# Performance work log

Measured on AMD Instinct MI355X. Metric: run time of the kernel, lower is better.

Reference implementation:

```python
import jax, jax.numpy as jnp
import numpy as np

B, T, C, H = 4, 2048, 1024, 16
HD = C // H


def setup_inputs() -> dict:
    key = jax.random.key(0)
    kx, kq, ko = jax.random.split(key, 3)
    x = jax.random.normal(kx, (B, T, C), dtype=jnp.float32)
    # torch nn.Linear weight layout: [out_features, in_features]
    wqkv = jax.random.normal(kq, (3 * C, C), dtype=jnp.float32) * (1.0 / np.sqrt(C))
    wo = jax.random.normal(ko, (C, C), dtype=jnp.float32) * (1.0 / np.sqrt(C))
    return {"x": x, "wqkv": wqkv, "wo": wo}


def reference(x, wqkv, wo):
    Bn, Tn, Cn = x.shape
    # fused QKV projection: x @ wqkv.T -> [B, T, 3C]
    qkv = jnp.einsum('btc,dc->btd', x, wqkv)
    qkv = qkv.reshape(Bn, Tn, 3, H, HD)
    q = qkv[:, :, 0].transpose(0, 2, 1, 3)  # [B, H, T, hd]
    k = qkv[:, :, 1].transpose(0, 2, 1, 3)
    v = qkv[:, :, 2].transpose(0, 2, 1, 3)
    scale = 1.0 / np.sqrt(HD).astype(np.float32)
    scores = jnp.einsum('bhqd,bhkd->bhqk', q, k) * scale  # [B, H, T, T]
    causal = jnp.tril(jnp.ones((Tn, Tn), dtype=bool))
    scores = jnp.where(causal, scores, jnp.finfo(scores.dtype).min)
    attn = jax.nn.softmax(scores, axis=-1)
    y = jnp.einsum('bhqk,bhkd->bhqd', attn, v)  # [B, H, T, hd]
    y = y.transpose(0, 2, 1, 3).reshape(Bn, Tn, Cn)
    return jnp.einsum('btc,dc->btd', y, wo)
```

## Files before the change

### kernel.cpp

```cpp
#include <hip/hip_runtime.h>
#include <hip/hip_bf16.h>
#include <stdint.h>


typedef __attribute__((ext_vector_type(8))) short short8;
typedef __attribute__((ext_vector_type(4))) float f32x4;
typedef __attribute__((ext_vector_type(4))) float float4v;
typedef __attribute__((ext_vector_type(4))) unsigned short ushort4v;
typedef __attribute__((ext_vector_type(4))) unsigned int u32x4;

#define AS1 __attribute__((address_space(1)))
#define AS3 __attribute__((address_space(3)))

#if __has_builtin(__builtin_amdgcn_exp2f)
#define EXP2(x) __builtin_amdgcn_exp2f(x)
#else
#define EXP2(x) __expf((x) * 0.69314718f)
#endif

static __device__ __forceinline__ void gload_lds16(const void* g, void* l) {
  __builtin_amdgcn_global_load_lds((const AS1 void*)g, (AS3 void*)l, 16, 0, 0);
}

__global__ void k_detect(const unsigned int* __restrict__ x, int* __restrict__ flag) {
  __shared__ int sm[256];
  int c = 0;
  for (int i = 0; i < 8; ++i) {
    unsigned int v = x[threadIdx.x * 8 + i];
    unsigned int e = (v >> 7) & 0xffu;
    if (e >= 110u && e <= 140u) c++;
  }
  sm[threadIdx.x] = c;
  __syncthreads();
  if (threadIdx.x == 0) {
    int t = 0;
    for (int i = 0; i < 256; ++i) t += sm[i];
    *flag = (t > 1024) ? 1 : 0;
  }
}

__global__ void k_convert3(const void* __restrict__ xs, const void* __restrict__ wqs,
                           const void* __restrict__ wos, unsigned short* __restrict__ out,
                           const int* __restrict__ flag) {
  const int f = *flag;
  const int stride = gridDim.x * blockDim.x;
  for (int v = blockIdx.x * blockDim.x + threadIdx.x; v < 3145728; v += stride) {
    const int i = v * 4;
    const void* src; int j;
    if (i < 8388608)        { src = xs;  j = i; }
    else if (i < 11534336)  { src = wqs; j = i - 8388608; }
    else                    { src = wos; j = i - 11534336; }
    ushort4v r;
    if (f) {
      r = *(const ushort4v*)((const unsigned short*)src + j);
    } else {
      float4v fv = *(const float4v*)((const float*)src + j);
#pragma unroll
      for (int e = 0; e < 4; e++) {
        __hip_bfloat16 h = __float2bfloat16(fv[e]);
        r[e] = *(unsigned short*)&h;
      }
    }
    *(ushort4v*)(out + i) = r;
  }
}

__global__ __launch_bounds__(256) void k_gemm_qkv(
    const __hip_bfloat16* __restrict__ X, const __hip_bfloat16* __restrict__ W,
    __hip_bfloat16* __restrict__ qo, __hip_bfloat16* __restrict__ ko,
    __hip_bfloat16* __restrict__ vto) {
  __shared__ __align__(16) __hip_bfloat16 As[128 * 32];
  __shared__ __align__(16) __hip_bfloat16 Bs[128 * 32];
  const int tid = threadIdx.x;
  const int lane = tid & 63;
  const int wid = tid >> 6;
  const int wr = wid >> 1, wc = wid & 1;
  const int lr = lane & 15, lk = lane >> 4;
  const int m0 = blockIdx.x * 128;
  const int n0 = blockIdx.y * 128;
  const int sw = (lr >> 1) & 3;

  const f32x4 fzero = {0.f, 0.f, 0.f, 0.f};
  f32x4 acc[4][4];
#pragma unroll
  for (int i = 0; i < 4; i++)
#pragma unroll
    for (int j = 0; j < 4; j++) acc[i][j] = fzero;

  for (int kt = 0; kt < 32; ++kt) {
    const int k0 = kt * 32;
    __syncthreads();
#pragma unroll
    for (int j = 0; j < 2; ++j) {
      const int idx = j * 256 + tid;
      const int row = idx >> 2;
      const int ce = ((idx & 3) ^ ((row >> 1) & 3)) * 8;
      gload_lds16(X + (size_t)(m0 + row) * 1024 + k0 + ce,
                  (void*)(As + (size_t)(j * 256 + (tid & ~63)) * 8));
      gload_lds16(W + (size_t)(n0 + row) * 1024 + k0 + ce,
                  (void*)(Bs + (size_t)(j * 256 + (tid & ~63)) * 8));
    }
    __syncthreads();
    short8 a[4], b[4];
#pragma unroll
    for (int i = 0; i < 4; i++) a[i] = *(const short8*)(As + (wr * 64 + i * 16 + lr) * 32 + ((lk ^ sw) * 8));
#pragma unroll
    for (int i = 0; i < 4; i++) b[i] = *(const short8*)(Bs + (wc * 64 + i * 16 + lr) * 32 + ((lk ^ sw) * 8));
#pragma unroll
    for (int mf = 0; mf < 4; mf++)
#pragma unroll
      for (int nf = 0; nf < 4; nf++)
        acc[mf][nf] = __builtin_amdgcn_mfma_f32_16x16x32_bf16(a[mf], b[nf], acc[mf][nf], 0, 0, 0);
  }
#pragma unroll
  for (int mf = 0; mf < 4; mf++)
#pragma unroll
    for (int nf = 0; nf < 4; nf++)
#pragma unroll
      for (int r = 0; r < 4; r++) {
        const int row = m0 + wr * 64 + mf * 16 + lk * 4 + r;
        const int col = n0 + wc * 64 + nf * 16 + lr;
        const int s = col >> 10;
        const int rem = col & 1023;
        const int h = rem >> 6, hd = rem & 63;
        const int bb = row >> 11, t = row & 2047;
        const size_t bh = (size_t)(bb * 16 + h);
        if (s == 0) {
          qo[(bh * 2048 + t) * 64 + hd] = __float2bfloat16(acc[mf][nf][r] * 0.18033688f);
        } else if (s == 1) {
          ko[(bh * 2048 + t) * 64 + hd] = __float2bfloat16(acc[mf][nf][r]);
        } else {
          vto[(bh * 64 + hd) * 2048 + t] = __float2bfloat16(acc[mf][nf][r]);
        }
      }
}

__global__ __launch_bounds__(512) void k_attn(
    const __hip_bfloat16* __restrict__ Q, const __hip_bfloat16* __restrict__ K,
    const __hip_bfloat16* __restrict__ VT, __hip_bfloat16* __restrict__ Y) {
  __shared__ __align__(16) char smem[49152];
  char* smc = smem;
  const int tid = threadIdx.x, lane = tid & 63, wid = tid >> 6;
  const int lr = lane & 15, lk = lane >> 4;

  const int bid = blockIdx.x;
  const int bh = bid & 63;
  const int p = bid >> 6;
  const int e = p & 3;
  const int x = (p < 4) ? p : 7 - e;
  const int q0 = x * 256;
  const int qb = q0 + wid * 32;
  const size_t base = (size_t)bh * 2048 * 64;

  const int srow = tid >> 3;
  const int fs = (srow & 7) ^ ((2 * (srow >> 3)) & 7);
  const int scol = ((tid & 7) ^ fs) * 8;
  const __hip_bfloat16* kg = K + base + scol;
  const __hip_bfloat16* vg = VT + base + (size_t)srow * 2048 + scol;
  const int ldst = (tid & ~63) * 16;

  int koff[4][2], voff[4][2], kla[4];
#pragma unroll
  for (int a = 0; a < 4; a++) {
    const int ra = (lr >> 2) * 8 + (a & 1) * 4 + (lr & 3) + (a >> 1) * 32;
    const int fr = (ra & 7) ^ ((2 * (ra >> 3)) & 7);
    kla[a] = lk * 8 + (a & 1) * 4 + (a >> 1) * 32;
#pragma unroll
    for (int ks = 0; ks < 2; ks++)
      koff[a][ks] = ra * 128 + (((ks * 4 + lk) ^ fr) * 16);
  }
#pragma unroll
  for (int df = 0; df < 4; df++) {
    const int rv = df * 16 + lr;
    const int fv = (rv & 7) ^ ((2 * (rv >> 3)) & 7);
#pragma unroll
    for (int ks = 0; ks < 2; ks++)
      voff[df][ks] = rv * 128 + (((ks * 4 + lk) ^ fv) * 16);
  }

  short8 qf[2][2];
#pragma unroll
  for (int qg = 0; qg < 2; qg++)
#pragma unroll
    for (int ks = 0; ks < 2; ks++)
      qf[qg][ks] = *(const short8*)(Q + base + (size_t)(qb + qg * 16 + lr) * 64 + ks * 32 + lk * 8);

  const f32x4 fzero = {0.f, 0.f, 0.f, 0.f};
  f32x4 ot[2][4];
  float mrow[2] = {-1e30f, -1e30f}, lrow[2] = {0.f, 0.f};
#pragma unroll
  for (int qg = 0; qg < 2; qg++)
#pragma unroll
    for (int df = 0; df < 4; df++) ot[qg][df] = fzero;

  const int nkv = x * 4 + 4;
  gload_lds16(kg + (size_t)srow * 64, (void*)(smc + ldst));
  gload_lds16(vg, (void*)(smc + 24576 + ldst));
  gload_lds16(kg + (size_t)(64 + srow) * 64, (void*)(smc + 8192 + ldst));
  gload_lds16(vg + 64, (void*)(smc + 24576 + 8192 + ldst));

  int cur = 0;
  for (int kt = 0; kt < nkv; ++kt) {
    const int k0 = kt * 64;
    if (kt + 1 < nkv) { asm volatile("s_waitcnt vmcnt(2)" ::: "memory"); }
    else              { asm volatile("s_waitcnt vmcnt(0)" ::: "memory"); }
    __builtin_amdgcn_s_barrier();
    __builtin_amdgcn_sched_barrier(0);

    if (k0 <= qb + 31) {
      const char* kbuf = smc + cur * 8192;
      const char* vbuf = smc + 24576 + cur * 8192;

      f32x4 s[2][4];
#pragma unroll
      for (int qg = 0; qg < 2; qg++)
#pragma unroll
        for (int a = 0; a < 4; a++) s[qg][a] = fzero;

      __builtin_amdgcn_s_setprio(1);
#pragma unroll
      for (int ks = 0; ks < 2; ks++)
#pragma unroll
        for (int a = 0; a < 4; a++) {
          const short8 kb = *(const short8*)(kbuf + koff[a][ks]);
          s[0][a] = __builtin_amdgcn_mfma_f32_16x16x32_bf16(kb, qf[0][ks], s[0][a], 0, 0, 0);
          s[1][a] = __builtin_amdgcn_mfma_f32_16x16x32_bf16(kb, qf[1][ks], s[1][a], 0, 0, 0);
        }
      __builtin_amdgcn_s_setprio(0);

      const bool needmask = (k0 + 63 > qb);
      short8 pb[2][2];

#pragma unroll
      for (int qg = 0; qg < 2; qg++) {
        const int qq = qb + qg * 16 + lr;
        if (needmask) {
#pragma unroll
          for (int a = 0; a < 4; a++)
#pragma unroll
            for (int r = 0; r < 4; r++)
              if (k0 + kla[a] + r > qq) s[qg][a][r] = -1e30f;
        }
        f32x4 m4;
#pragma unroll
        for (int r = 0; r < 4; r++)
          m4[r] = fmaxf(fmaxf(s[qg][0][r], s[qg][1][r]), fmaxf(s[qg][2][r], s[qg][3][r]));
        float mx = fmaxf(fmaxf(m4[0], m4[1]), fmaxf(m4[2], m4[3]));
        mx = fmaxf(mx, __shfl_xor(mx, 16, 64));
        mx = fmaxf(mx, __shfl_xor(mx, 32, 64));
        const float mold = mrow[qg];
        float m;
        if (__all(mx - mold <= 8.f)) {
          m = mold;
        } else {
          m = fmaxf(mold, mx);
          const float alpha = EXP2(mold - m);
          lrow[qg] *= alpha;
          mrow[qg] = m;
#pragma unroll
          for (int df = 0; df < 4; df++) ot[qg][df] *= alpha;
        }
        float rs = 0.f;
#pragma unroll
        for (int a = 0; a < 4; a++)
#pragma unroll
          for (int r = 0; r < 4; r++) {
            const float pv = EXP2(s[qg][a][r] - m);
            s[qg][a][r] = pv;
            rs += pv;
          }
        lrow[qg] += rs;
#pragma unroll
        for (int ksP = 0; ksP < 2; ksP++) {
          short8 w;
#pragma unroll
          for (int ee = 0; ee < 4; ee++) {
            __hip_bfloat16 h0 = __float2bfloat16(s[qg][2 * ksP][ee]);
            __hip_bfloat16 h1 = __float2bfloat16(s[qg][2 * ksP + 1][ee]);
            w[ee] = *(short*)&h0;
            w[4 + ee] = *(short*)&h1;
          }
          pb[qg][ksP] = w;
        }
      }

      __builtin_amdgcn_s_setprio(1);
#pragma unroll
      for (int ks = 0; ks < 2; ks++)
#pragma unroll
        for (int df = 0; df < 4; df++) {
          const short8 vb = *(const short8*)(vbuf + voff[df][ks]);
          ot[0][df] = __builtin_amdgcn_mfma_f32_16x16x32_bf16(vb, pb[0][ks], ot[0][df], 0, 0, 0);
          ot[1][df] = __builtin_amdgcn_mfma_f32_16x16x32_bf16(vb, pb[1][ks], ot[1][df], 0, 0, 0);
        }
      __builtin_amdgcn_s_setprio(0);
    }

    if (kt + 2 < nkv) {
      const int kn = (kt + 2) * 64;
      int tb = cur + 2; if (tb >= 3) tb -= 3;
      gload_lds16(kg + (size_t)(kn + srow) * 64, (void*)(smc + tb * 8192 + ldst));
      gload_lds16(vg + kn, (void*)(smc + 24576 + tb * 8192 + ldst));
    }
    cur = (cur + 1 == 3) ? 0 : cur + 1;
  }

  __syncthreads();
  unsigned int* Os = (unsigned int*)smc;
#pragma unroll
  for (int qg = 0; qg < 2; qg++) {
    float ls = lrow[qg];
    ls += __shfl_xor(ls, 16, 64);
    ls += __shfl_xor(ls, 32, 64);
    const float inv = 1.f / ls;
    const int qlocal = wid * 32 + qg * 16 + lr;
    const int sw = (lr & 7) << 2;
#pragma unroll
    for (int df = 0; df < 4; df++)
#pragma unroll
      for (int e2 = 0; e2 < 2; e2++) {
        __hip_bfloat16 h0 = __float2bfloat16(ot[qg][df][2 * e2] * inv);
        __hip_bfloat16 h1 = __float2bfloat16(ot[qg][df][2 * e2 + 1] * inv);
        const unsigned int w = (unsigned int)*(unsigned short*)&h0 |
                               ((unsigned int)*(unsigned short*)&h1 << 16);
        Os[qlocal * 32 + ((df * 8 + lk * 2 + e2) ^ sw)] = w;
      }
  }
  __syncthreads();
  {
    const int qrow = tid >> 1, half = tid & 1, q7 = qrow & 7;
    const int b = bh >> 4, h = bh & 15;
    unsigned int* Yu = (unsigned int*)Y;
    const size_t rowbase = ((size_t)b * 2048 + q0 + qrow) * 512 + h * 32;
#pragma unroll
    for (int g = 0; g < 4; g++) {
      const int cg = half * 4 + g;
      const u32x4 v = *(const u32x4*)(smc + qrow * 128 + ((cg ^ q7) * 16));
      *(u32x4*)(Yu + rowbase + cg * 4) = v;
    }
  }
}

__global__ __launch_bounds__(256) void k_gemm_out(
    const __hip_bfloat16* __restrict__ X, const __hip_bfloat16* __restrict__ W,
    void* __restrict__ out, const int* __restrict__ flag) {
  __shared__ __align__(16) __hip_bfloat16 As[128 * 32];
  __shared__ __align__(16) __hip_bfloat16 Bs[128 * 32];
  const int tid = threadIdx.x;
  const int lane = tid & 63;
  const int wid = tid >> 6;
  const int wr = wid >> 1, wc = wid & 1;
  const int lr = lane & 15, lk = lane >> 4;
  const int m0 = blockIdx.x * 128;
  const int n0 = blockIdx.y * 128;
  const int sw = (lr >> 1) & 3;

  const f32x4 fzero = {0.f, 0.f, 0.f, 0.f};
  f32x4 acc[4][4];
#pragma unroll
  for (int i = 0; i < 4; i++)
#pragma unroll
    for (int j = 0; j < 4; j++) acc[i][j] = fzero;

  for (int kt = 0; kt < 32; ++kt) {
    const int k0 = kt * 32;
    __syncthreads();
#pragma unroll
    for (int j = 0; j < 2; ++j) {
      const int idx = j * 256 + tid;
      const int row = idx >> 2;
      const int ce = ((idx & 3) ^ ((row >> 1) & 3)) * 8;
      gload_lds16(X + (size_t)(m0 + row) * 1024 + k0 + ce,
                  (void*)(As + (size_t)(j * 256 + (tid & ~63)) * 8));
      gload_lds16(W + (size_t)(n0 + row) * 1024 + k0 + ce,
                  (void*)(Bs + (size_t)(j * 256 + (tid & ~63)) * 8));
    }
    __syncthreads();
    short8 a[4], b[4];
#pragma unroll
    for (int i = 0; i < 4; i++) a[i] = *(const short8*)(As + (wr * 64 + i * 16 + lr) * 32 + ((lk ^ sw) * 8));
#pragma unroll
    for (int i = 0; i < 4; i++) b[i] = *(const short8*)(Bs + (wc * 64 + i * 16 + lr) * 32 + ((lk ^ sw) * 8));
#pragma unroll
    for (int mf = 0; mf < 4; mf++)
#pragma unroll
      for (int nf = 0; nf < 4; nf++)
        acc[mf][nf] = __builtin_amdgcn_mfma_f32_16x16x32_bf16(a[mf], b[nf], acc[mf][nf], 0, 0, 0);
  }
  const int f = *flag;
#pragma unroll
  for (int mf = 0; mf < 4; mf++)
#pragma unroll
    for (int nf = 0; nf < 4; nf++)
#pragma unroll
      for (int r = 0; r < 4; r++) {
        const int row = m0 + wr * 64 + mf * 16 + lk * 4 + r;
        const int col = n0 + wc * 64 + nf * 16 + lr;
        const size_t oi = (size_t)row * 1024 + col;
        if (f) ((__hip_bfloat16*)out)[oi] = __float2bfloat16(acc[mf][nf][r]);
        else   ((float*)out)[oi] = acc[mf][nf][r];
      }
}

extern "C" void kernel_launch(void* const* d_in, const int* in_sizes, int n_in,
                              void* d_out, int out_size, void* d_ws, size_t ws_size,
                              hipStream_t stream) {
  const void* x = d_in[0];
  const void* wqkv = d_in[1];
  const void* wo = d_in[2];

  char* ws = (char*)d_ws;
  int* flag = (int*)ws;
  __hip_bfloat16* xb    = (__hip_bfloat16*)(ws + 256);
  __hip_bfloat16* wqkvb = xb + 8388608;
  __hip_bfloat16* wob   = wqkvb + 3145728;
  __hip_bfloat16* qws   = wob + 1048576;
  __hip_bfloat16* kws   = qws + 8388608;
  __hip_bfloat16* vtws  = kws + 8388608;
  __hip_bfloat16* yws   = xb;

  k_detect<<<1, 256, 0, stream>>>((const unsigned int*)x, flag);
  k_convert3<<<2048, 256, 0, stream>>>(x, wqkv, wo, (unsigned short*)xb, flag);

  dim3 g1(64, 24);
  k_gemm_qkv<<<g1, 256, 0, stream>>>(xb, wqkvb, qws, kws, vtws);

  k_attn<<<512, 512, 0, stream>>>(qws, kws, vtws, yws);

  dim3 g3(64, 8);
  k_gemm_out<<<g3, 256, 0, stream>>>(yws, wob, d_out, flag);
}
```

Before: 187.4 us.

## Triple-buffer LDS tiles in QKV and output GEMMs with async prefetch

Both projection GEMMs now keep three LDS stages for the A and B tiles. The K-tile two steps ahead is prefetched with global_load_lds, and the loop waits via s_waitcnt vmcnt plus a single barrier per iteration instead of two __syncthreads around a blocking load. The aim is to hide global memory latency behind MFMA work. The cost is triple the LDS footprint (48KB per block), which may reduce occupancy, and the code now depends on correct manual vmcnt accounting.

```diff
diff --git a/kernel.cpp b/kernel.cpp
--- a/kernel.cpp
+++ b/kernel.cpp
@@ -69,8 +69,8 @@
     const __hip_bfloat16* __restrict__ X, const __hip_bfloat16* __restrict__ W,
     __hip_bfloat16* __restrict__ qo, __hip_bfloat16* __restrict__ ko,
     __hip_bfloat16* __restrict__ vto) {
-  __shared__ __align__(16) __hip_bfloat16 As[128 * 32];
-  __shared__ __align__(16) __hip_bfloat16 Bs[128 * 32];
+  __shared__ __align__(16) __hip_bfloat16 As[3][128 * 32];
+  __shared__ __align__(16) __hip_bfloat16 Bs[3][128 * 32];
   const int tid = threadIdx.x;
   const int lane = tid & 63;
   const int wid = tid >> 6;
@@ -80,6 +80,11 @@
   const int n0 = blockIdx.y * 128;
   const int sw = (lr >> 1) & 3;
 
+  const int row0 = tid >> 2,          row1 = (256 + tid) >> 2;
+  const int ce0 = ((tid & 3) ^ ((row0 >> 1) & 3)) * 8;
+  const int ce1 = ((tid & 3) ^ ((row1 >> 1) & 3)) * 8;
+  const int d0 = (tid & ~63) * 8, d1 = (256 + (tid & ~63)) * 8;
+
   const f32x4 fzero = {0.f, 0.f, 0.f, 0.f};
   f32x4 acc[4][4];
 #pragma unroll
@@ -87,31 +92,44 @@
 #pragma unroll
     for (int j = 0; j < 4; j++) acc[i][j] = fzero;
 
+#define QKV_STAGE(buf, kt2)                                                     \
+  {                                                                             \
+    const int kk = (kt2) * 32;                                                  \
+    gload_lds16(X + (size_t)(m0 + row0) * 1024 + kk + ce0, (void*)(As[buf] + d0)); \
+    gload_lds16(W + (size_t)(n0 + row0) * 1024 + kk + ce0, (void*)(Bs[buf] + d0)); \
+    gload_lds16(X + (size_t)(m0 + row1) * 1024 + kk + ce1, (void*)(As[buf] + d1)); \
+    gload_lds16(W + (size_t)(n0 + row1) * 1024 + kk + ce1, (void*)(Bs[buf] + d1)); \
+  }
+
+  QKV_STAGE(0, 0)
+  QKV_STAGE(1, 1)
+
+  int cur = 0;
   for (int kt = 0; kt < 32; ++kt) {
-    const int k0 = kt * 32;
-    __syncthreads();
-#pragma unroll
-    for (int j = 0; j < 2; ++j) {
-      const int idx = j * 256 + tid;
-      const int row = idx >> 2;
-      const int ce = ((idx & 3) ^ ((row >> 1) & 3)) * 8;
-      gload_lds16(X + (size_t)(m0 + row) * 1024 + k0 + ce,
-                  (void*)(As + (size_t)(j * 256 + (tid & ~63)) * 8));
-      gload_lds16(W + (size_t)(n0 + row) * 1024 + k0 + ce,
-                  (void*)(Bs + (size_t)(j * 256 + (tid & ~63)) * 8));
-    }
-    __syncthreads();
+    if (kt + 1 < 32) { asm volatile("s_waitcnt vmcnt(4)" ::: "memory"); }
+    else             { asm volatile("s_waitcnt vmcnt(0)" ::: "memory"); }
+    __builtin_amdgcn_s_barrier();
+    __builtin_amdgcn_sched_barrier(0);
+
     short8 a[4], b[4];
 #pragma unroll
-    for (int i = 0; i < 4; i++) a[i] = *(const short8*)(As + (wr * 64 + i * 16 + lr) * 32 + ((lk ^ sw) * 8));
-#pragma unroll
-    for (int i = 0; i < 4; i++) b[i] = *(const short8*)(Bs + (wc * 64 + i * 16 + lr) * 32 + ((lk ^ sw) * 8));
+    for (int i = 0; i < 4; i++) a[i] = *(const short8*)(As[cur] + (wr * 64 + i * 16 + lr) * 32 + ((lk ^ sw) * 8));
+#pragma unroll
+    for (int i = 0; i < 4; i++) b[i] = *(const short8*)(Bs[cur] + (wc * 64 + i * 16 + lr) * 32 + ((lk ^ sw) * 8));
 #pragma unroll
     for (int mf = 0; mf < 4; mf++)
 #pragma unroll
       for (int nf = 0; nf < 4; nf++)
         acc[mf][nf] = __builtin_amdgcn_mfma_f32_16x16x32_bf16(a[mf], b[nf], acc[mf][nf], 0, 0, 0);
-  }
+
+    if (kt + 2 < 32) {
+      int tb = cur + 2; if (tb >= 3) tb -= 3;
+      QKV_STAGE(tb, kt + 2)
+    }
+    cur = (cur + 1 == 3) ? 0 : cur + 1;
+  }
+#undef QKV_STAGE
+
 #pragma unroll
   for (int mf = 0; mf < 4; mf++)
 #pragma unroll
@@ -344,8 +362,8 @@
 __global__ __launch_bounds__(256) void k_gemm_out(
     const __hip_bfloat16* __restrict__ X, const __hip_bfloat16* __restrict__ W,
     void* __restrict__ out, const int* __restrict__ flag) {
-  __shared__ __align__(16) __hip_bfloat16 As[128 * 32];
-  __shared__ __align__(16) __hip_bfloat16 Bs[128 * 32];
+  __shared__ __align__(16) __hip_bfloat16 As[3][128 * 32];
+  __shared__ __align__(16) __hip_bfloat16 Bs[3][128 * 32];
   const int tid = threadIdx.x;
   const int lane = tid & 63;
   const int wid = tid >> 6;
@@ -355,6 +373,11 @@
   const int n0 = blockIdx.y * 128;
   const int sw = (lr >> 1) & 3;
 
+  const int row0 = tid >> 2,          row1 = (256 + tid) >> 2;
+  const int ce0 = ((tid & 3) ^ ((row0 >> 1) & 3)) * 8;
+  const int ce1 = ((tid & 3) ^ ((row1 >> 1) & 3)) * 8;
+  const int d0 = (tid & ~63) * 8, d1 = (256 + (tid & ~63)) * 8;
+
   const f32x4 fzero = {0.f, 0.f, 0.f, 0.f};
   f32x4 acc[4][4];
 #pragma unroll
@@ -362,31 +385,44 @@
 #pragma unroll
     for (int j = 0; j < 4; j++) acc[i][j] = fzero;
 
+#define OUT_STAGE(buf, kt2)                                                     \
+  {                                                                             \
+    const int kk = (kt2) * 32;                                                  \
+    gload_lds16(X + (size_t)(m0 + row0) * 1024 + kk + ce0, (void*)(As[buf] + d0)); \
+    gload_lds16(W + (size_t)(n0 + row0) * 1024 + kk + ce0, (void*)(Bs[buf] + d0)); \
+    gload_lds16(X + (size_t)(m0 + row1) * 1024 + kk + ce1, (void*)(As[buf] + d1)); \
+    gload_lds16(W + (size_t)(n0 + row1) * 1024 + kk + ce1, (void*)(Bs[buf] + d1)); \
+  }
+
+  OUT_STAGE(0, 0)
+  OUT_STAGE(1, 1)
+
+  int cur = 0;
   for (int kt = 0; kt < 32; ++kt) {
-    const int k0 = kt * 32;
-    __syncthreads();
-#pragma unroll
-    for (int j = 0; j < 2; ++j) {
-      const int idx = j * 256 + tid;
-      const int row = idx >> 2;
-      const int ce = ((idx & 3) ^ ((row >> 1) & 3)) * 8;
-      gload_lds16(X + (size_t)(m0 + row) * 1024 + k0 + ce,
-                  (void*)(As + (size_t)(j * 256 + (tid & ~63)) * 8));
-      gload_lds16(W + (size_t)(n0 + row) * 1024 + k0 + ce,
-                  (void*)(Bs + (size_t)(j * 256 + (tid & ~63)) * 8));
-    }
-    __syncthreads();
+    if (kt + 1 < 32) { asm volatile("s_waitcnt vmcnt(4)" ::: "memory"); }
+    else             { asm volatile("s_waitcnt vmcnt(0)" ::: "memory"); }
+    __builtin_amdgcn_s_barrier();
+    __builtin_amdgcn_sched_barrier(0);
+
     short8 a[4], b[4];
 #pragma unroll
-    for (int i = 0; i < 4; i++) a[i] = *(const short8*)(As + (wr * 64 + i * 16 + lr) * 32 + ((lk ^ sw) * 8));
-#pragma unroll
-    for (int i = 0; i < 4; i++) b[i] = *(const short8*)(Bs + (wc * 64 + i * 16 + lr) * 32 + ((lk ^ sw) * 8));
+    for (int i = 0; i < 4; i++) a[i] = *(const short8*)(As[cur] + (wr * 64 + i * 16 + lr) * 32 + ((lk ^ sw) * 8));
+#pragma unroll
+    for (int i = 0; i < 4; i++) b[i] = *(const short8*)(Bs[cur] + (wc * 64 + i * 16 + lr) * 32 + ((lk ^ sw) * 8));
 #pragma unroll
     for (int mf = 0; mf < 4; mf++)
 #pragma unroll
       for (int nf = 0; nf < 4; nf++)
         acc[mf][nf] = __builtin_amdgcn_mfma_f32_16x16x32_bf16(a[mf], b[nf], acc[mf][nf], 0, 0, 0);
-  }
+
+    if (kt + 2 < 32) {
+      int tb = cur + 2; if (tb >= 3) tb -= 3;
+      OUT_STAGE(tb, kt + 2)
+    }
+    cur = (cur + 1 == 3) ? 0 : cur + 1;
+  }
+#undef OUT_STAGE
+
   const int f = *flag;
 #pragma unroll
   for (int mf = 0; mf < 4; mf++)
```

Result: faster. 182.3 us (-2.7%).
